# Kernel optimization log

Measured on AMD Instinct MI355X. Metric: run time of the kernel, lower is better.

The kernel has to match this reference:

```python
import jax, jax.numpy as jnp
import numpy as np

D_MODEL = 512
NUM_HEADS = 8
DK = D_MODEL // NUM_HEADS
SCALE = DK ** -0.5


def setup_inputs() -> dict:
    key = jax.random.key(0)
    ks = jax.random.split(key, 8)
    B, S = 4, 8192
    q = jax.random.normal(ks[0], (B, S, D_MODEL), dtype=jnp.float32)
    k = jax.random.normal(ks[1], (B, S, D_MODEL), dtype=jnp.float32)
    v = jax.random.normal(ks[2], (B, S, D_MODEL), dtype=jnp.float32)
    init = (2.0 / D_MODEL) ** 0.5  # rough kaiming-like scale
    W_q = jax.random.normal(ks[3], (D_MODEL, D_MODEL), dtype=jnp.float32) * init
    W_k = jax.random.normal(ks[4], (D_MODEL, D_MODEL), dtype=jnp.float32) * init
    W_v = jax.random.normal(ks[5], (D_MODEL, D_MODEL), dtype=jnp.float32) * init
    W_o = jax.random.normal(ks[6], (D_MODEL, D_MODEL), dtype=jnp.float32) * init
    b_o = jax.random.normal(ks[7], (D_MODEL,), dtype=jnp.float32) * 0.01
    return {"q": q, "k": k, "v": v, "W_q": W_q, "W_k": W_k, "W_v": W_v, "W_o": W_o, "b_o": b_o}


def reference(q, k, v, W_q, W_k, W_v, W_o, b_o):
    B, S, C = q.shape
    H, dk = NUM_HEADS, DK
    # projections (torch Linear: x @ W.T)
    qh = (q @ W_q.T).reshape(B, S, H, dk).transpose(0, 2, 1, 3)  # [B,H,S,dk]
    kh = (k @ W_k.T).reshape(B, S, H, dk).transpose(0, 2, 1, 3)
    vh = (v @ W_v.T).reshape(B, S, H, dk).transpose(0, 2, 1, 3)
    # linear attention: G = (K^T * scale) @ V  -> [B,H,dk,dk]
    G = jnp.einsum('bhsd,bhse->bhde', kh * SCALE, vh)
    # out = (Q * scale) @ G  -> [B,H,S,dk]
    out = jnp.einsum('bhsd,bhde->bhse', qh * SCALE, G)
    out = out.transpose(0, 2, 1, 3).reshape(B, S, C)
    return out @ W_o.T + b_o
```

## Files before the change

kernel.cpp:

```cpp
#include <hip/hip_runtime.h>
#include <hip/hip_bf16.h>


typedef __attribute__((ext_vector_type(4))) float f32x4;
typedef __attribute__((ext_vector_type(8))) short short8;

#define DEVI __device__ __forceinline__

DEVI unsigned short f2bf(float f) {
  unsigned int u = __builtin_bit_cast(unsigned int, f);
  u += 0x7fffu + ((u >> 16) & 1u);
  return (unsigned short)(u >> 16);
}
DEVI float bf2f(unsigned short s) {
  unsigned int u = ((unsigned int)s) << 16;
  return __builtin_bit_cast(float, u);
}
DEVI short8 pack8(f32x4 a, f32x4 b) {
  short8 r;
#pragma unroll
  for (int i = 0; i < 4; ++i) { r[i] = (short)f2bf(a[i]); r[i + 4] = (short)f2bf(b[i]); }
  return r;
}

__global__ __launch_bounds__(256, 2) void bigm_kernel(const float* __restrict__ kmat,
                                                      const float* __restrict__ vmat,
                                                      unsigned short* __restrict__ Mpart) {
  __shared__ __align__(16) unsigned short Vt[2][128 * 40];
  __shared__ __align__(16) unsigned short Kt[2][128 * 40];
  const int t = threadIdx.x;
  const int bid = blockIdx.x;
  const int xcd = bid & 7, jj = bid >> 3;
  const int p = ((jj >> 4) << 3) | xcd;
  const int tile = jj & 15;
  const int b = p >> 4, split = p & 15;
  const int ti = tile >> 2, tj = tile & 3;
  const int cp0 = ti * 128, ck0 = tj * 128;

  const int lane = t & 63, w = t >> 6;
  const int fr = lane & 15, fg = lane >> 4;
  const int wm = (w >> 1) * 64, wn = (w & 1) * 64;

  const int half = t >> 7;
  const int u = t & 127;
  const int cg = u & 31, sg = u >> 5;
  const float* srcg = (half ? kmat : vmat)
                    + ((size_t)b * 8192 + (size_t)split * 512) * 512
                    + (half ? ck0 : cp0) + cg * 4;
  unsigned short* dstl = (half ? &Kt[0][0] : &Vt[0][0]);
  const int wbase = cg * 4 * 40 + ((sg ^ (cg & 3)) << 3);

  f32x4 rA[8], rB[8];
  auto gloadA = [&](int sbase) {
    const float* pp = srcg + (size_t)(sbase + sg * 8) * 512;
#pragma unroll
    for (int j = 0; j < 8; ++j) rA[j] = *(const f32x4*)(pp + j * 512);
  };
  auto gloadB = [&](int sbase) {
    const float* pp = srcg + (size_t)(sbase + sg * 8) * 512;
#pragma unroll
    for (int j = 0; j < 8; ++j) rB[j] = *(const f32x4*)(pp + j * 512);
  };
  auto lwriteA = [&](int buf) {
    unsigned short* d = dstl + buf * (128 * 40) + wbase;
#pragma unroll
    for (int ci = 0; ci < 4; ++ci) {
      short8 wv;
#pragma unroll
      for (int j = 0; j < 8; ++j) wv[j] = (short)f2bf(rA[j][ci]);
      *(short8*)(d + ci * 40) = wv;
    }
  };
  auto lwriteB = [&](int buf) {
    unsigned short* d = dstl + buf * (128 * 40) + wbase;
#pragma unroll
    for (int ci = 0; ci < 4; ++ci) {
      short8 wv;
#pragma unroll
      for (int j = 0; j < 8; ++j) wv[j] = (short)f2bf(rB[j][ci]);
      *(short8*)(d + ci * 40) = wv;
    }
  };

  f32x4 acc[4][4] = {};
  const int key = fr >> 2;
  auto mfma_phase = [&](int cbuf) {
    short8 fa[4], fb[4];
#pragma unroll
    for (int i = 0; i < 4; ++i) {
      fa[i] = *(const short8*)&Vt[cbuf][(wm + i * 16 + fr) * 40 + ((fg ^ key) << 3)];
      fb[i] = *(const short8*)&Kt[cbuf][(wn + i * 16 + fr) * 40 + ((fg ^ key) << 3)];
    }
#pragma unroll
    for (int i = 0; i < 4; ++i)
#pragma unroll
      for (int j = 0; j < 4; ++j)
        acc[i][j] = __builtin_amdgcn_mfma_f32_16x16x32_bf16(fa[i], fb[j], acc[i][j], 0, 0, 0);
  };

  gloadA(0);
  lwriteA(0);
  gloadB(32);
  __syncthreads();

  for (int it = 0; it < 8; ++it) {
    const int s0 = it * 2;
    if (it < 7) gloadA((s0 + 2) * 32);
    mfma_phase(0);
    lwriteB(1);
    __syncthreads();
    if (it < 7) gloadB((s0 + 3) * 32);
    mfma_phase(1);
    if (it < 7) lwriteA(0);
    __syncthreads();
  }

  unsigned short* gp = Mpart + (size_t)p * 262144;
#pragma unroll
  for (int i = 0; i < 4; ++i)
#pragma unroll
    for (int j = 0; j < 4; ++j)
#pragma unroll
      for (int r2 = 0; r2 < 4; ++r2)
        gp[(size_t)(cp0 + wm + i * 16 + fg * 4 + r2) * 512 + ck0 + wn + j * 16 + fr] =
            f2bf(acc[i][j][r2]);
}

__global__ __launch_bounds__(256) void mred_kernel(const unsigned short* __restrict__ Mpart,
                                                   unsigned short* __restrict__ Msum) {
  const int base = (blockIdx.x * 256 + threadIdx.x) * 8;
  const int b = base >> 18;
  const int r = base & 262143;
  const unsigned short* src = Mpart + (size_t)(b * 16) * 262144 + r;
  float s[8] = {};
#pragma unroll
  for (int c = 0; c < 16; ++c) {
    short8 u = *(const short8*)(src + (size_t)c * 262144);
#pragma unroll
    for (int j = 0; j < 8; ++j) s[j] += bf2f((unsigned short)u[j]);
  }
  short8 o;
#pragma unroll
  for (int j = 0; j < 8; ++j) o[j] = (short)f2bf(s[j]);
  *(short8*)(Msum + base) = o;
}

__global__ __launch_bounds__(256, 3) void stepa_kernel(const float* __restrict__ Wk,
                                                       const unsigned short* __restrict__ Msum,
                                                       unsigned short* __restrict__ P) {
  __shared__ __align__(16) unsigned short Ab[2][128 * 40];
  __shared__ __align__(16) unsigned short Bb[2][128 * 40];
  const int t = threadIdx.x;
  const int n0 = blockIdx.x * 128;
  const int m0 = blockIdx.y * 128;
  const int b = blockIdx.z;
  const int lane = t & 63, w = t >> 6;
  const int wm = (w >> 1) * 64, wn = (w & 1) * 64;
  const int fr = lane & 15, fg = lane >> 4;
  const int sr = t >> 2;
  const int sk = (t & 3) * 8;

  const float* pAg = Wk + (size_t)(m0 + sr) * 512 + sk;
  const unsigned short* pBg = Msum + (size_t)b * 262144 + (size_t)(n0 + sr) * 512 + sk;

  f32x4 acc[4][4] = {};
  f32x4 a0, a1, a2, a3;
  short8 sb0, sb1;

  a0 = *(const f32x4*)(pAg);         a1 = *(const f32x4*)(pAg + 4);
  a2 = *(const f32x4*)(pAg + 32768); a3 = *(const f32x4*)(pAg + 32772);
  sb0 = *(const short8*)(pBg);
  sb1 = *(const short8*)(pBg + 32768);
  *(short8*)&Ab[0][sr * 40 + sk] = pack8(a0, a1);
  *(short8*)&Ab[0][(sr + 64) * 40 + sk] = pack8(a2, a3);
  *(short8*)&Bb[0][sr * 40 + sk] = sb0;
  *(short8*)&Bb[0][(sr + 64) * 40 + sk] = sb1;
  __syncthreads();

  for (int step = 0; step < 16; ++step) {
    const int cur = step & 1;
    if (step < 15) {
      const int k1 = (step + 1) * 32;
      a0 = *(const f32x4*)(pAg + k1);         a1 = *(const f32x4*)(pAg + k1 + 4);
      a2 = *(const f32x4*)(pAg + k1 + 32768); a3 = *(const f32x4*)(pAg + k1 + 32772);
      sb0 = *(const short8*)(pBg + k1);
      sb1 = *(const short8*)(pBg + k1 + 32768);
    }
    short8 afr[4], bfr[4];
#pragma unroll
    for (int i = 0; i < 4; ++i) {
      afr[i] = *(const short8*)&Ab[cur][(wm + i * 16 + fr) * 40 + fg * 8];
      bfr[i] = *(const short8*)&Bb[cur][(wn + i * 16 + fr) * 40 + fg * 8];
    }
#pragma unroll
    for (int i = 0; i < 4; ++i)
#pragma unroll
      for (int j = 0; j < 4; ++j)
        acc[i][j] = __builtin_amdgcn_mfma_f32_16x16x32_bf16(afr[i], bfr[j], acc[i][j], 0, 0, 0);
    if (step < 15) {
      const int nxt = cur ^ 1;
      *(short8*)&Ab[nxt][sr * 40 + sk] = pack8(a0, a1);
      *(short8*)&Ab[nxt][(sr + 64) * 40 + sk] = pack8(a2, a3);
      *(short8*)&Bb[nxt][sr * 40 + sk] = sb0;
      *(short8*)&Bb[nxt][(sr + 64) * 40 + sk] = sb1;
    }
    __syncthreads();
  }
#pragma unroll
  for (int i = 0; i < 4; ++i)
#pragma unroll
    for (int j = 0; j < 4; ++j)
#pragma unroll
      for (int r = 0; r < 4; ++r) {
        const int row = m0 + wm + i * 16 + fg * 4 + r;
        const int col = n0 + wn + j * 16 + fr;
        P[((size_t)b * 512 + row) * 512 + col] = f2bf(acc[i][j][r]);
      }
}

__global__ __launch_bounds__(64) void stepb_kernel(const unsigned short* __restrict__ P,
                                                   const float* __restrict__ Wv,
                                                   float* __restrict__ Gsum) {
  __shared__ __align__(16) unsigned short Ao[64 * 40];
  __shared__ __align__(16) unsigned short Bo[64 * 40];
  const int t = threadIdx.x;
  const int h = blockIdx.x;
  const int b = blockIdx.y;
  const int fr = t & 15, fg = t >> 4;
  f32x4 acc[4][4] = {};
  for (int step = 0; step < 16; ++step) {
    const int k0 = step * 32;
    const unsigned short* pa = P + ((size_t)b * 512 + h * 64 + t) * 512 + k0;
#pragma unroll
    for (int i = 0; i < 4; ++i) *(short8*)&Ao[t * 40 + i * 8] = *(const short8*)(pa + i * 8);
    const float* pb = Wv + (size_t)(h * 64 + t) * 512 + k0;
#pragma unroll
    for (int i = 0; i < 4; ++i) {
      f32x4 x0 = *(const f32x4*)(pb + i * 8);
      f32x4 x1 = *(const f32x4*)(pb + i * 8 + 4);
      *(short8*)&Bo[t * 40 + i * 8] = pack8(x0, x1);
    }
    __syncthreads();
    short8 afr[4], bfr[4];
#pragma unroll
    for (int i = 0; i < 4; ++i) {
      afr[i] = *(const short8*)&Ao[(i * 16 + fr) * 40 + fg * 8];
      bfr[i] = *(const short8*)&Bo[(i * 16 + fr) * 40 + fg * 8];
    }
#pragma unroll
    for (int i = 0; i < 4; ++i)
#pragma unroll
      for (int j = 0; j < 4; ++j)
        acc[i][j] = __builtin_amdgcn_mfma_f32_16x16x32_bf16(afr[i], bfr[j], acc[i][j], 0, 0, 0);
    __syncthreads();
  }
  float* gout = Gsum + (size_t)(b * 8 + h) * 4096;
#pragma unroll
  for (int i = 0; i < 4; ++i)
#pragma unroll
    for (int j = 0; j < 4; ++j)
#pragma unroll
      for (int r = 0; r < 4; ++r)
        gout[(i * 16 + fg * 4 + r) * 64 + (j * 16 + fr)] = acc[i][j][r] * 0.015625f;
}

__global__ __launch_bounds__(256) void t3_kernel(const float* __restrict__ Wq,
                                                 const float* __restrict__ Gsum,
                                                 unsigned short* __restrict__ T3) {
  __shared__ float Wl[64][64];
  __shared__ float Gl[64][64];
  const int t = threadIdx.x;
  const int c0 = blockIdx.x * 64;
  const int h = blockIdx.y;
  const int b = blockIdx.z;
  const int dd = t >> 2;
  const int c4 = (t & 3) * 16;
  const float* wp = Wq + (size_t)(h * 64 + dd) * 512 + c0 + c4;
  const float* gp = Gsum + (size_t)(b * 8 + h) * 4096 + dd * 64 + c4;
#pragma unroll
  for (int i = 0; i < 4; ++i) {
    *(f32x4*)&Wl[dd][c4 + i * 4] = *(const f32x4*)(wp + i * 4);
    *(f32x4*)&Gl[dd][c4 + i * 4] = *(const f32x4*)(gp + i * 4);
  }
  __syncthreads();
  const int cl0 = (t >> 4) * 4;
  const int e0 = (t & 15) * 4;
  float acc[4][4] = {};
  for (int d = 0; d < 64; ++d) {
    f32x4 wv = *(const f32x4*)&Wl[d][cl0];
    f32x4 gv = *(const f32x4*)&Gl[d][e0];
#pragma unroll
    for (int i = 0; i < 4; ++i)
#pragma unroll
      for (int j = 0; j < 4; ++j)
        acc[i][j] += wv[i] * gv[j];
  }
#pragma unroll
  for (int i = 0; i < 4; ++i)
#pragma unroll
    for (int j = 0; j < 4; ++j)
      T3[((size_t)b * 512 + c0 + cl0 + i) * 512 + h * 64 + e0 + j] = f2bf(acc[i][j]);
}

__global__ __launch_bounds__(64) void wc_kernel(const float* __restrict__ Wo,
                                                const unsigned short* __restrict__ T3,
                                                unsigned short* __restrict__ WcT) {
  __shared__ __align__(16) unsigned short Ao[64 * 48];
  __shared__ __align__(16) unsigned short Bo[64 * 48];
  const int t = threadIdx.x;
  const int n0 = blockIdx.x * 64;
  const int c0 = blockIdx.y * 64;
  const int b = blockIdx.z;
  const int fr = t & 15, fg = t >> 4;
  f32x4 acc[4][4] = {};
  for (int step = 0; step < 16; ++step) {
    const int k0 = step * 32;
    const float* pa = Wo + (size_t)(n0 + t) * 512 + k0;
    unsigned short tmp[32];
#pragma unroll
    for (int i = 0; i < 8; ++i) {
      f32x4 vv = *(const f32x4*)(pa + i * 4);
#pragma unroll
      for (int j = 0; j < 4; ++j) tmp[i * 4 + j] = f2bf(vv[j]);
    }
#pragma unroll
    for (int i = 0; i < 4; ++i) *(short8*)&Ao[t * 48 + i * 8] = *(const short8*)&tmp[i * 8];
    const unsigned short* pb = T3 + ((size_t)b * 512 + c0 + t) * 512 + k0;
#pragma unroll
    for (int i = 0; i < 4; ++i) *(short8*)&Bo[t * 48 + i * 8] = *(const short8*)(pb + i * 8);
    __syncthreads();
    short8 afr[4], bfr[4];
#pragma unroll
    for (int i = 0; i < 4; ++i) {
      afr[i] = *(const short8*)&Ao[(i * 16 + fr) * 48 + fg * 8];
      bfr[i] = *(const short8*)&Bo[(i * 16 + fr) * 48 + fg * 8];
    }
#pragma unroll
    for (int i = 0; i < 4; ++i)
#pragma unroll
      for (int j = 0; j < 4; ++j)
        acc[i][j] = __builtin_amdgcn_mfma_f32_16x16x32_bf16(afr[i], bfr[j], acc[i][j], 0, 0, 0);
    __syncthreads();
  }
#pragma unroll
  for (int i = 0; i < 4; ++i)
#pragma unroll
    for (int j = 0; j < 4; ++j)
#pragma unroll
      for (int r = 0; r < 4; ++r)
        WcT[((size_t)b * 512 + n0 + i * 16 + fg * 4 + r) * 512 + c0 + j * 16 + fr] =
            f2bf(acc[i][j][r]);
}

__global__ __launch_bounds__(256, 3) void out_kernel(const float* __restrict__ q,
                                                     const unsigned short* __restrict__ WcT,
                                                     const float* __restrict__ bo,
                                                     float* __restrict__ Out) {
  __shared__ __align__(16) unsigned short Ab[2][128 * 40];
  __shared__ __align__(16) unsigned short Bb[2][128 * 40];
  const int t = threadIdx.x;
  const int bid = blockIdx.x;
  const int xcd = bid & 7, idx = bid >> 3;
  const int mt = xcd * 32 + (idx >> 2);
  const int nt = idx & 3;
  const int m0 = mt * 128, n0 = nt * 128;
  const unsigned short* Wc = WcT + ((size_t)(m0 >> 13)) * 512 * 512;
  const int lane = t & 63, w = t >> 6;
  const int wm = (w >> 1) * 64, wn = (w & 1) * 64;
  const int fr = lane & 15, fg = lane >> 4;
  const int sr = t >> 2;
  const int sk = (t & 3) * 8;

  const float* pAg = q + (size_t)(m0 + sr) * 512 + sk;
  const unsigned short* pBg = Wc + (size_t)(n0 + sr) * 512 + sk;

  f32x4 aA[4], aB[4];
  short8 bA[2], bB[2];
  auto gloadA = [&](int k) {
    aA[0] = *(const f32x4*)(pAg + k);         aA[1] = *(const f32x4*)(pAg + k + 4);
    aA[2] = *(const f32x4*)(pAg + k + 32768); aA[3] = *(const f32x4*)(pAg + k + 32772);
    bA[0] = *(const short8*)(pBg + k);
    bA[1] = *(const short8*)(pBg + k + 32768);
  };
  auto gloadB = [&](int k) {
    aB[0] = *(const f32x4*)(pAg + k);         aB[1] = *(const f32x4*)(pAg + k + 4);
    aB[2] = *(const f32x4*)(pAg + k + 32768); aB[3] = *(const f32x4*)(pAg + k + 32772);
    bB[0] = *(const short8*)(pBg + k);
    bB[1] = *(const short8*)(pBg + k + 32768);
  };
  auto lwriteA = [&](int buf) {
    *(short8*)&Ab[buf][sr * 40 + sk] = pack8(aA[0], aA[1]);
    *(short8*)&Ab[buf][(sr + 64) * 40 + sk] = pack8(aA[2], aA[3]);
    *(short8*)&Bb[buf][sr * 40 + sk] = bA[0];
    *(short8*)&Bb[buf][(sr + 64) * 40 + sk] = bA[1];
  };
  auto lwriteB = [&](int buf) {
    *(short8*)&Ab[buf][sr * 40 + sk] = pack8(aB[0], aB[1]);
    *(short8*)&Ab[buf][(sr + 64) * 40 + sk] = pack8(aB[2], aB[3]);
    *(short8*)&Bb[buf][sr * 40 + sk] = bB[0];
    *(short8*)&Bb[buf][(sr + 64) * 40 + sk] = bB[1];
  };

  f32x4 acc[4][4] = {};
  auto mfma_phase = [&](int cbuf) {
    short8 afr[4], bfr[4];
#pragma unroll
    for (int i = 0; i < 4; ++i) {
      afr[i] = *(const short8*)&Ab[cbuf][(wm + i * 16 + fr) * 40 + fg * 8];
      bfr[i] = *(const short8*)&Bb[cbuf][(wn + i * 16 + fr) * 40 + fg * 8];
    }
#pragma unroll
    for (int i = 0; i < 4; ++i)
#pragma unroll
      for (int j = 0; j < 4; ++j)
        acc[i][j] = __builtin_amdgcn_mfma_f32_16x16x32_bf16(afr[i], bfr[j], acc[i][j], 0, 0, 0);
  };

  gloadA(0);
  lwriteA(0);
  gloadB(32);
  __syncthreads();

  for (int it = 0; it < 8; ++it) {
    const int s0 = it * 2;
    if (it < 7) gloadA((s0 + 2) * 32);
    mfma_phase(0);
    lwriteB(1);
    __syncthreads();
    if (it < 7) gloadB((s0 + 3) * 32);
    mfma_phase(1);
    if (it < 7) lwriteA(0);
    __syncthreads();
  }

  float bias[4];
#pragma unroll
  for (int j = 0; j < 4; ++j) bias[j] = bo[n0 + wn + j * 16 + fr];
#pragma unroll
  for (int i = 0; i < 4; ++i)
#pragma unroll
    for (int j = 0; j < 4; ++j)
#pragma unroll
      for (int r = 0; r < 4; ++r) {
        const int row = m0 + wm + i * 16 + fg * 4 + r;
        const int col = n0 + wn + j * 16 + fr;
        Out[(size_t)row * 512 + col] = acc[i][j][r] + bias[j];
      }
}

extern "C" void kernel_launch(void* const* d_in, const int* in_sizes, int n_in,
                              void* d_out, int out_size, void* d_ws, size_t ws_size,
                              hipStream_t stream) {
  const float* q  = (const float*)d_in[0];
  const float* k  = (const float*)d_in[1];
  const float* v  = (const float*)d_in[2];
  const float* Wq = (const float*)d_in[3];
  const float* Wk = (const float*)d_in[4];
  const float* Wv = (const float*)d_in[5];
  const float* Wo = (const float*)d_in[6];
  const float* bo = (const float*)d_in[7];
  float* Out = (float*)d_out;

  unsigned short* Mpart = (unsigned short*)d_out;
  char* ws = (char*)d_ws;
  unsigned short* Msum = (unsigned short*)ws;
  unsigned short* P    = (unsigned short*)(ws + (size_t)2 * 1048576);
  float* Gsum          = (float*)(ws + (size_t)4 * 1048576);
  unsigned short* T3   = (unsigned short*)(ws + (size_t)5 * 1048576);
  unsigned short* WcT  = (unsigned short*)(ws + (size_t)7 * 1048576);

  bigm_kernel<<<1024, 256, 0, stream>>>(k, v, Mpart);
  mred_kernel<<<512, 256, 0, stream>>>(Mpart, Msum);
  stepa_kernel<<<dim3(4, 4, 4), 256, 0, stream>>>(Wk, Msum, P);
  stepb_kernel<<<dim3(8, 4), 64, 0, stream>>>(P, Wv, Gsum);
  t3_kernel<<<dim3(8, 8, 4), 256, 0, stream>>>(Wq, Gsum, T3);
  wc_kernel<<<dim3(8, 8, 4), 64, 0, stream>>>(Wo, T3, WcT);
  out_kernel<<<1024, 256, 0, stream>>>(q, WcT, bo, Out);
}
```

Before: 161.6 us.

## Single register prefetch buffer in bigm kernel and raise occupancy target

Replaces the two register staging sets (rA/rB) with one prefetch buffer in a simple double-buffered LDS loop with one barrier per step. It raises the launch-bounds occupancy hint from 2 to 4 blocks per CU and uses the compiler's native bf16 conversion instead of a manual round-to-nearest-even. The aim is lower register pressure so more waves fit per CU and hide global-load latency better. In exchange, less load data is in flight per thread, and forcing the compiler to fit 4 blocks could cause spills with the 64 accumulator floats. LDS use of about 40KB per block may also cap residency below 4.

New measurement: 158.1 us, median of 2. -2.2%, faster.

```diff
diff --git a/kernel.cpp b/kernel.cpp
--- a/kernel.cpp
+++ b/kernel.cpp
@@ -8,9 +8,8 @@
 #define DEVI __device__ __forceinline__
 
 DEVI unsigned short f2bf(float f) {
-  unsigned int u = __builtin_bit_cast(unsigned int, f);
-  u += 0x7fffu + ((u >> 16) & 1u);
-  return (unsigned short)(u >> 16);
+  __bf16 h = (__bf16)f;
+  return __builtin_bit_cast(unsigned short, h);
 }
 DEVI float bf2f(unsigned short s) {
   unsigned int u = ((unsigned int)s) << 16;
@@ -23,7 +22,7 @@
   return r;
 }
 
-__global__ __launch_bounds__(256, 2) void bigm_kernel(const float* __restrict__ kmat,
+__global__ __launch_bounds__(256, 4) void bigm_kernel(const float* __restrict__ kmat,
                                                       const float* __restrict__ vmat,
                                                       unsigned short* __restrict__ Mpart) {
   __shared__ __align__(16) unsigned short Vt[2][128 * 40];
@@ -50,71 +49,47 @@
   unsigned short* dstl = (half ? &Kt[0][0] : &Vt[0][0]);
   const int wbase = cg * 4 * 40 + ((sg ^ (cg & 3)) << 3);
 
-  f32x4 rA[8], rB[8];
-  auto gloadA = [&](int sbase) {
+  f32x4 r[8];
+  auto gload = [&](int sbase) {
     const float* pp = srcg + (size_t)(sbase + sg * 8) * 512;
 #pragma unroll
-    for (int j = 0; j < 8; ++j) rA[j] = *(const f32x4*)(pp + j * 512);
-  };
-  auto gloadB = [&](int sbase) {
-    const float* pp = srcg + (size_t)(sbase + sg * 8) * 512;
-#pragma unroll
-    for (int j = 0; j < 8; ++j) rB[j] = *(const f32x4*)(pp + j * 512);
-  };
-  auto lwriteA = [&](int buf) {
+    for (int j = 0; j < 8; ++j) r[j] = *(const f32x4*)(pp + j * 512);
+  };
+  auto lwrite = [&](int buf) {
     unsigned short* d = dstl + buf * (128 * 40) + wbase;
 #pragma unroll
     for (int ci = 0; ci < 4; ++ci) {
       short8 wv;
 #pragma unroll
-      for (int j = 0; j < 8; ++j) wv[j] = (short)f2bf(rA[j][ci]);
+      for (int j = 0; j < 8; ++j) wv[j] = (short)f2bf(r[j][ci]);
       *(short8*)(d + ci * 40) = wv;
     }
   };
-  auto lwriteB = [&](int buf) {
-    unsigned short* d = dstl + buf * (128 * 40) + wbase;
-#pragma unroll
-    for (int ci = 0; ci < 4; ++ci) {
-      short8 wv;
-#pragma unroll
-      for (int j = 0; j < 8; ++j) wv[j] = (short)f2bf(rB[j][ci]);
-      *(short8*)(d + ci * 40) = wv;
-    }
-  };
 
   f32x4 acc[4][4] = {};
+
+  gload(0);
+  lwrite(0);
+  __syncthreads();
+
   const int key = fr >> 2;
-  auto mfma_phase = [&](int cbuf) {
+  for (int step = 0; step < 16; ++step) {
+    const int cur = step & 1;
+    if (step < 15) gload((step + 1) * 32);
     short8 fa[4], fb[4];
 #pragma unroll
     for (int i = 0; i < 4; ++i) {
-      fa[i] = *(const short8*)&Vt[cbuf][(wm + i * 16 + fr) * 40 + ((fg ^ key) << 3)];
-      fb[i] = *(const short8*)&Kt[cbuf][(wn + i * 16 + fr) * 40 + ((fg ^ key) << 3)];
+      fa[i] = *(const short8*)&Vt[cur][(wm + i * 16 + fr) * 40 + ((fg ^ key) << 3)];
+      fb[i] = *(const short8*)&Kt[cur][(wn + i * 16 + fr) * 40 + ((fg ^ key) << 3)];
     }
 #pragma unroll
     for (int i = 0; i < 4; ++i)
 #pragma unroll
       for (int j = 0; j < 4; ++j)
         acc[i][j] = __builtin_amdgcn_mfma_f32_16x16x32_bf16(fa[i], fb[j], acc[i][j], 0, 0, 0);
-  };
-
-  gloadA(0);
-  lwriteA(0);
-  gloadB(32);
-  __syncthreads();
-
-  for (int it = 0; it < 8; ++it) {
-    const int s0 = it * 2;
-    if (it < 7) gloadA((s0 + 2) * 32);
-    mfma_phase(0);
-    lwriteB(1);
-    __syncthreads();
-    if (it < 7) gloadB((s0 + 3) * 32);
-    mfma_phase(1);
-    if (it < 7) lwriteA(0);
-    __syncthreads();
-  }
-
+    if (step < 15) lwrite(cur ^ 1);
+    __syncthreads();
+  }
   unsigned short* gp = Mpart + (size_t)p * 262144;
 #pragma unroll
   for (int i = 0; i < 4; ++i)
```
